# Kernel optimization log

Measured on AMD Instinct MI355X. Metric: run time of the kernel, lower is better.

Reference implementation:

```python
import jax, jax.numpy as jnp
import numpy as np

FS = 50000000.0
PI = jnp.pi


def _scale_matrix(alpha, kW, n_pad):
    """kW x kW matrix equal to torch linear-interp (align_corners=False)
    kW -> N -> kW with N = round(kW / clamp(alpha, 0.001)), N bounded by n_pad."""
    a = jnp.maximum(alpha, 0.001)
    N = jnp.clip(jnp.round(kW / a), 1, n_pad).astype(jnp.int32)
    Nf = N.astype(jnp.float32)
    eye_k = jnp.eye(kW, dtype=jnp.float32)
    eye_n = jnp.eye(n_pad, dtype=jnp.float32)
    # down-sample matrix D: length kW -> N (rows j >= N masked to 0)
    j = jnp.arange(n_pad, dtype=jnp.float32)
    c = jnp.maximum((j + 0.5) * (kW / Nf) - 0.5, 0.0)
    i0f = jnp.floor(c)
    w1 = c - i0f
    i0 = jnp.clip(i0f.astype(jnp.int32), 0, kW - 1)
    i1 = jnp.minimum(i0 + 1, kW - 1)
    D = (1.0 - w1)[:, None] * eye_k[i0] + w1[:, None] * eye_k[i1]
    D = D * (jnp.arange(n_pad) < N)[:, None]
    # up-sample matrix U: length N -> kW (reads only cols < N)
    i = jnp.arange(kW, dtype=jnp.float32)
    c2 = jnp.maximum((i + 0.5) * (Nf / kW) - 0.5, 0.0)
    j0 = jnp.floor(c2).astype(jnp.int32)
    j1 = jnp.minimum(j0 + 1, N - 1)
    w2 = c2 - j0.astype(jnp.float32)
    U = (1.0 - w2)[:, None] * eye_n[j0] + w2[:, None] * eye_n[j1]
    return U @ D  # [kW, kW]


def _mix_phase(w, phi):
    # w: [B,OC,2,1,kW], phi: [B,kW]; complex rotation of (I,Q) channel pair
    I, Q = w[:, :, 0, 0, :], w[:, :, 1, 0, :]
    c, sn = jnp.cos(phi)[:, None, :], jnp.sin(phi)[:, None, :]
    return jnp.stack([I * c - Q * sn, I * sn + Q * c], axis=2)[:, :, :, None, :]


def _steered_kernels(z, s, base_w, B):
    OC, IC, _, kW = base_w.shape
    n_pad = 2 * kW
    sf = jnp.nan_to_num(s)
    act = z > 0
    pick = lambda idx, neutral: jnp.where(act[:, idx], sf[:, idx], neutral)
    wB = jnp.broadcast_to(base_w[None], (B, OC, IC, 1, kW))
    # SCALE (PERTURB_ORDER idx 1)
    alpha = pick(1, 1.0)
    M = jax.vmap(lambda a: _scale_matrix(a, kW, n_pad))(alpha)  # [B,kW,kW]
    wB = jnp.einsum('bij,bocuj->bocui', M, wB)
    # CFO (idx 0) then CHIRP (idx 4): sequential phase rotations = summed phase
    n = jnp.arange(kW, dtype=jnp.float32)
    phi = 2.0 * PI * pick(0, 0.0)[:, None] * n[None, :] / FS
    t = n / FS
    phi = phi + PI * pick(4, 0.0)[:, None] * (t ** 2)[None, :]
    wB = _mix_phase(wB, phi)
    # GAIN (idx 2)
    wB = pick(2, 1.0)[:, None, None, None, None] * wB
    # SHIFT (idx 3): per-sample circular roll, out[i] = in[(i - s) mod kW]
    sh = jnp.round(pick(3, 0.0)).astype(jnp.int32)
    idx = (jnp.arange(kW)[None, :] - sh[:, None]) % kW  # [B,kW]
    idx = jnp.broadcast_to(idx[:, None, None, None, :], wB.shape)
    wB = jnp.take_along_axis(wB, idx, axis=-1)
    return wB  # [B,OC,2,1,kW]


def reference(x, z, s, base_w):
    B, IC, _, L = x.shape
    OC, _, _, kW = base_w.shape
    wB = _steered_kernels(z, s, base_w, B)
    xG = x.reshape(1, B * IC, 1, L)
    wG = wB.reshape(B * OC, IC, 1, kW)
    y = jax.lax.conv_general_dilated(
        xG, wG, window_strides=(1, 1), padding=[(0, 0), (kW // 2, kW // 2)],
        dimension_numbers=('NCHW', 'OIHW', 'NCHW'), feature_group_count=B)
    return y.reshape(B, OC, 1, L)


def setup_inputs() -> dict:
    key = jax.random.key(0)
    ks = jax.random.split(key, 4)
    B, OC, IC, kW, L = 32, 64, 2, 65, 65536
    x = jax.random.normal(ks[0], (B, IC, 1, L), dtype=jnp.float32)
    base_w = jax.random.normal(ks[1], (OC, IC, 1, kW), dtype=jnp.float32) * 0.1
    z = jax.random.randint(ks[2], (B, 5), 0, 2).astype(jnp.int32)
    u = jax.random.uniform(ks[3], (B, 5), dtype=jnp.float32)
    f0 = (u[:, 0] * 2.0 - 1.0) * 1.0e5         # CFO in +/-100 kHz
    alpha = 0.75 + u[:, 1] * 0.65               # SCALE in [0.75, 1.4]
    gain = 0.5 + u[:, 2]                        # GAIN in [0.5, 1.5]
    shift = jnp.round((u[:, 3] * 2.0 - 1.0) * 3.0)  # SHIFT integer in [-3, 3]
    chirp = (u[:, 4] * 2.0 - 1.0) * 1.0e12      # CHIRP rate
    s = jnp.stack([f0, alpha, gain, shift, chirp], axis=1)
    return {"x": x, "z": z, "s": s, "base_w": base_w}
```

## Files before the change

### kernel.cpp

```cpp
#include <hip/hip_runtime.h>
#include <math.h>

#define KW 65
#define L_LEN 65536
#define B_N 32
#define OC_N 64
#define KPAD 160
#define SEC 80
#define LT 256
#define NT 8
#define LGRP (LT*NT)
#define XBASE 344

typedef __attribute__((ext_vector_type(8))) short short8;
typedef __attribute__((ext_vector_type(4))) float f32x4;

__device__ __forceinline__ unsigned short f2bf(float f) {
    unsigned u = __builtin_bit_cast(unsigned, f);
    unsigned r = u + 0x7FFFu + ((u >> 16) & 1u);
    return (unsigned short)(r >> 16);
}

__device__ __forceinline__ float nan0(float v) {
    if (isnan(v)) return 0.0f;
    if (isinf(v)) return v > 0.0f ? 3.4028234663852886e38f : -3.4028234663852886e38f;
    return v;
}

__device__ __forceinline__ void barrier_lds() {
    __builtin_amdgcn_fence(__ATOMIC_RELEASE, "workgroup", "local");
    __builtin_amdgcn_s_barrier();
    __builtin_amdgcn_fence(__ATOMIC_ACQUIRE, "workgroup", "local");
}

__global__ __launch_bounds__(256) void steer_weights(
        const int* __restrict__ z, const float* __restrict__ s,
        const float* __restrict__ bw, unsigned short* __restrict__ wpk) {
    const float PI = 3.14159265358979323846f;
    const float FS = 50000000.0f;
    int b = blockIdx.x;
    int t = threadIdx.x;

    const int*   zb = z + b * 5;
    const float* sb = s + b * 5;
    float f0    = (zb[0] > 0) ? nan0(sb[0]) : 0.0f;
    float alpha = (zb[1] > 0) ? nan0(sb[1]) : 1.0f;
    float gain  = (zb[2] > 0) ? nan0(sb[2]) : 1.0f;
    float shf   = (zb[3] > 0) ? nan0(sb[3]) : 0.0f;
    float chirp = (zb[4] > 0) ? nan0(sb[4]) : 0.0f;

    float a = fmaxf(alpha, 0.001f);
    float Nf_raw = rintf(65.0f / a);
    int   N  = (int)fminf(fmaxf(Nf_raw, 1.0f), 130.0f);
    float Nf = (float)N;
    int   sh = (int)rintf(shf);

    __shared__ float rw[OC_N][2][KW];
    __shared__ float cph[KW], sph[KW];
    __shared__ int   j0t[KW], j1t[KW];
    __shared__ float w2t[KW];
    __shared__ int   i0t[130], i1t[130];
    __shared__ float w1t[130];

    if (t < KW) {
        float n  = (float)t;
        float tt = n / FS;
        float phi = 2.0f * PI * f0 * n / FS + PI * chirp * tt * tt;
        cph[t] = cosf(phi);
        sph[t] = sinf(phi);
        float c2  = fmaxf(((float)t + 0.5f) * (Nf / 65.0f) - 0.5f, 0.0f);
        float j0f = floorf(c2);
        j0t[t] = (int)j0f;
        j1t[t] = min((int)j0f + 1, N - 1);
        w2t[t] = c2 - j0f;
    } else if (t < KW + 130) {
        int j = t - KW;
        float c   = fmaxf(((float)j + 0.5f) * (65.0f / Nf) - 0.5f, 0.0f);
        float i0f = floorf(c);
        int   i0  = min((int)i0f, KW - 1);
        i0t[j] = i0;
        i1t[j] = min(i0 + 1, KW - 1);
        w1t[j] = c - i0f;
    }
    __syncthreads();

    for (int item = t; item < 128 * KW; item += 256) {
        int row = item / KW, i = item % KW;
        const float* w = bw + row * KW;
        int j0 = j0t[i], j1 = j1t[i];
        float v0 = (1.0f - w1t[j0]) * w[i0t[j0]] + w1t[j0] * w[i1t[j0]];
        float v1 = (1.0f - w1t[j1]) * w[i0t[j1]] + w1t[j1] * w[i1t[j1]];
        rw[row >> 1][row & 1][i] = (1.0f - w2t[i]) * v0 + w2t[i] * v1;
    }
    __syncthreads();

    {
        int oc = t >> 2, q = t & 3;
        unsigned short* ob = wpk + ((size_t)b * OC_N + oc) * KPAD;
        int sh0 = ((sh % KW) + KW) % KW;
        int k0 = 17 * q, k1 = min(KW, k0 + 17);
        for (int k = k0; k < k1; ++k) {
            float I = rw[oc][0][k], Q = rw[oc][1][k];
            float cp = cph[k], sp = sph[k];
            float Ip = (I * cp - Q * sp) * gain;
            float Qp = (I * sp + Q * cp) * gain;
            int kk = k + sh0; if (kk >= KW) kk -= KW;
            ob[kk]       = f2bf(Ip);
            ob[SEC + kk] = f2bf(Qp);
        }
        if (q == 3) {
            for (int kk = KW; kk < SEC; ++kk) { ob[kk] = 0; ob[SEC + kk] = 0; }
        }
    }
}

__global__ __launch_bounds__(256, 3) void steer_conv_mfma(
        const float* __restrict__ x, const unsigned short* __restrict__ wpk,
        float* __restrict__ y) {
    int b   = blockIdx.y;
    int L0  = blockIdx.x * LGRP;
    int tid = threadIdx.x;
    int wv = tid >> 6, lane = tid & 63;
    int c = lane & 15, g = lane >> 4;
    int a = wv & 1, lsub = wv >> 1;

    __shared__ __align__(16) unsigned short xt[2][8][2][XBASE];

    short8 afr[2][5];
    #pragma unroll
    for (int ot = 0; ot < 2; ++ot) {
        const unsigned short* wb = wpk + ((size_t)b * OC_N + 32 * a + 16 * ot + c) * KPAD;
        #pragma unroll
        for (int s = 0; s < 5; ++s)
            afr[ot][s] = *(const short8*)(wb + 32 * s + 8 * g);
    }

    const float* xb = x + (size_t)b * 2 * L_LEN;

    bool isLoader = (tid >= 84);
    int lidx = tid - 84;
    int lch = lidx / 86, li4 = lidx % 86;

    int boff[5];
    #pragma unroll
    for (int s = 0; s < 5; ++s) {
        int k0 = 32 * s + 8 * g;
        int ch = (k0 >= SEC) ? 1 : 0;
        int t0 = k0 - SEC * ch;
        boff[s] = ch * XBASE + 128 * lsub + 8 * c + t0;
    }

    auto loadwin = [&](int l0) -> float4 {
        int gi = l0 - 32 + 4 * li4;
        float4 v;
        if (gi >= 0 && gi + 3 < L_LEN) {
            v = *(const float4*)(xb + (size_t)lch * L_LEN + gi);
        } else {
            float tmp[4];
            #pragma unroll
            for (int u = 0; u < 4; ++u) {
                int q = gi + u;
                tmp[u] = (q >= 0 && q < L_LEN) ? xb[(size_t)lch * L_LEN + q] : 0.0f;
            }
            v = make_float4(tmp[0], tmp[1], tmp[2], tmp[3]);
        }
        return v;
    };

    float4 v = make_float4(0.f, 0.f, 0.f, 0.f);
    if (isLoader) v = loadwin(L0);

    int cur = 0;
    for (int t = 0; t < NT; ++t) {
        int l0 = L0 + t * LT;
        if (isLoader) {
            unsigned r0 = (unsigned)f2bf(v.x) | ((unsigned)f2bf(v.y) << 16);
            unsigned r1 = (unsigned)f2bf(v.z) | ((unsigned)f2bf(v.w) << 16);
            *(uint2*)&xt[cur][0][lch][4 * li4] = make_uint2(r0, r1);
        }
        barrier_lds();
        if (tid < 84) {
            int ch = tid / 42, j = tid % 42;
            const unsigned* src = (const unsigned*)&xt[cur][0][ch][8 * j];
            unsigned d[8];
            #pragma unroll
            for (int i = 0; i < 8; ++i) d[i] = src[i];
            #pragma unroll
            for (int p = 1; p < 8; ++p) {
                int q = p >> 1;
                unsigned o[4];
                #pragma unroll
                for (int i = 0; i < 4; ++i)
                    o[i] = (p & 1) ? ((d[i + q] >> 16) | (d[i + q + 1] << 16)) : d[i + q];
                *(uint4*)&xt[cur][p][ch][8 * j] = make_uint4(o[0], o[1], o[2], o[3]);
            }
        } else if (t + 1 < NT) {
            int gi = L0 + (t + 1) * LT - 32 + 4 * li4;
            if (gi >= 0 && gi + 3 < L_LEN) {
                v = loadwin(l0 + LT);
            } else {
                v = loadwin(l0 + LT);
            }
        }
        barrier_lds();

        f32x4 acc[2][8];
        #pragma unroll
        for (int ot = 0; ot < 2; ++ot)
            #pragma unroll
            for (int p = 0; p < 8; ++p) acc[ot][p] = (f32x4){0.f, 0.f, 0.f, 0.f};

        #pragma unroll
        for (int p = 0; p < 8; ++p) {
            const unsigned short* xp = &xt[cur][p][0][0];
            #pragma unroll
            for (int s = 0; s < 5; ++s) {
                short8 bfr = *(const short8*)(xp + boff[s]);
                acc[0][p] = __builtin_amdgcn_mfma_f32_16x16x32_bf16(afr[0][s], bfr, acc[0][p], 0, 0, 0);
                acc[1][p] = __builtin_amdgcn_mfma_f32_16x16x32_bf16(afr[1][s], bfr, acc[1][p], 0, 0, 0);
            }
        }

        #pragma unroll
        for (int ot = 0; ot < 2; ++ot) {
            #pragma unroll
            for (int r = 0; r < 4; ++r) {
                int oc = 32 * a + 16 * ot + 4 * g + r;
                float* yr = y + ((size_t)b * OC_N + oc) * L_LEN + l0 + 128 * lsub + 8 * c;
                f32x4 lo = { acc[ot][0][r], acc[ot][1][r], acc[ot][2][r], acc[ot][3][r] };
                f32x4 hi = { acc[ot][4][r], acc[ot][5][r], acc[ot][6][r], acc[ot][7][r] };
                *(f32x4*)yr       = lo;
                *((f32x4*)yr + 1) = hi;
            }
        }
        cur ^= 1;
    }
}

extern "C" void kernel_launch(void* const* d_in, const int* in_sizes, int n_in,
                              void* d_out, int out_size, void* d_ws, size_t ws_size,
                              hipStream_t stream) {
    const float* x  = (const float*)d_in[0];
    const int*   z  = (const int*)d_in[1];
    const float* s  = (const float*)d_in[2];
    const float* bw = (const float*)d_in[3];
    float* y = (float*)d_out;
    unsigned short* wpk = (unsigned short*)d_ws;

    steer_weights<<<dim3(B_N), dim3(256), 0, stream>>>(z, s, bw, wpk);
    steer_conv_mfma<<<dim3(L_LEN / LGRP, B_N), dim3(256), 0, stream>>>(x, wpk, y);
}
```

Measured before the change: 153.1 us.

## Split weight steering across OC groups and raise conv occupancy bound

The weight-steering kernel now launches 8 blocks per batch, each handling 8 output channels, instead of one block per batch, so more CUs share that prologue work. The conv kernel's launch bounds go from 3 to 4 waves per SIMD, which may force more register pressure or spills. It also replaces the custom LDS-only fence barrier with __syncthreads and adds an interior-block fast path that skips bounds checks on the input loads. Each idea is small on its own, and together they touch both kernels.

```diff
diff --git a/kernel.cpp b/kernel.cpp
--- a/kernel.cpp
+++ b/kernel.cpp
@@ -27,19 +27,14 @@
     return v;
 }
 
-__device__ __forceinline__ void barrier_lds() {
-    __builtin_amdgcn_fence(__ATOMIC_RELEASE, "workgroup", "local");
-    __builtin_amdgcn_s_barrier();
-    __builtin_amdgcn_fence(__ATOMIC_ACQUIRE, "workgroup", "local");
-}
-
 __global__ __launch_bounds__(256) void steer_weights(
         const int* __restrict__ z, const float* __restrict__ s,
         const float* __restrict__ bw, unsigned short* __restrict__ wpk) {
     const float PI = 3.14159265358979323846f;
     const float FS = 50000000.0f;
-    int b = blockIdx.x;
-    int t = threadIdx.x;
+    int ocg = blockIdx.x;
+    int b   = blockIdx.y;
+    int t   = threadIdx.x;
 
     const int*   zb = z + b * 5;
     const float* sb = s + b * 5;
@@ -55,7 +50,7 @@
     float Nf = (float)N;
     int   sh = (int)rintf(shf);
 
-    __shared__ float rw[OC_N][2][KW];
+    __shared__ float rw[8][2][KW];
     __shared__ float cph[KW], sph[KW];
     __shared__ int   j0t[KW], j1t[KW];
     __shared__ float w2t[KW];
@@ -84,9 +79,9 @@
     }
     __syncthreads();
 
-    for (int item = t; item < 128 * KW; item += 256) {
+    for (int item = t; item < 16 * KW; item += 256) {
         int row = item / KW, i = item % KW;
-        const float* w = bw + row * KW;
+        const float* w = bw + (((ocg * 8 + (row >> 1)) * 2) + (row & 1)) * KW;
         int j0 = j0t[i], j1 = j1t[i];
         float v0 = (1.0f - w1t[j0]) * w[i0t[j0]] + w1t[j0] * w[i1t[j0]];
         float v1 = (1.0f - w1t[j1]) * w[i0t[j1]] + w1t[j1] * w[i1t[j1]];
@@ -94,27 +89,27 @@
     }
     __syncthreads();
 
-    {
-        int oc = t >> 2, q = t & 3;
-        unsigned short* ob = wpk + ((size_t)b * OC_N + oc) * KPAD;
-        int sh0 = ((sh % KW) + KW) % KW;
-        int k0 = 17 * q, k1 = min(KW, k0 + 17);
-        for (int k = k0; k < k1; ++k) {
-            float I = rw[oc][0][k], Q = rw[oc][1][k];
-            float cp = cph[k], sp = sph[k];
-            float Ip = (I * cp - Q * sp) * gain;
-            float Qp = (I * sp + Q * cp) * gain;
-            int kk = k + sh0; if (kk >= KW) kk -= KW;
-            ob[kk]       = f2bf(Ip);
-            ob[SEC + kk] = f2bf(Qp);
-        }
-        if (q == 3) {
-            for (int kk = KW; kk < SEC; ++kk) { ob[kk] = 0; ob[SEC + kk] = 0; }
-        }
-    }
-}
-
-__global__ __launch_bounds__(256, 3) void steer_conv_mfma(
+    int sh0 = ((sh % KW) + KW) % KW;
+    for (int item = t; item < 8 * KW; item += 256) {
+        int ocl = item / KW, k = item % KW;
+        unsigned short* ob = wpk + ((size_t)b * OC_N + ocg * 8 + ocl) * KPAD;
+        float I = rw[ocl][0][k], Q = rw[ocl][1][k];
+        float cp = cph[k], sp = sph[k];
+        float Ip = (I * cp - Q * sp) * gain;
+        float Qp = (I * sp + Q * cp) * gain;
+        int kk = k + sh0; if (kk >= KW) kk -= KW;
+        ob[kk]       = f2bf(Ip);
+        ob[SEC + kk] = f2bf(Qp);
+    }
+    for (int item = t; item < 8 * 30; item += 256) {
+        int ocl = item / 30, rem = item % 30;
+        int sec = rem / 15, kk = KW + rem % 15;
+        unsigned short* ob = wpk + ((size_t)b * OC_N + ocg * 8 + ocl) * KPAD;
+        ob[sec * SEC + kk] = 0;
+    }
+}
+
+__global__ __launch_bounds__(256, 4) void steer_conv_mfma(
         const float* __restrict__ x, const unsigned short* __restrict__ wpk,
         float* __restrict__ y) {
     int b   = blockIdx.y;
@@ -135,11 +130,11 @@
             afr[ot][s] = *(const short8*)(wb + 32 * s + 8 * g);
     }
 
-    const float* xb = x + (size_t)b * 2 * L_LEN;
-
     bool isLoader = (tid >= 84);
     int lidx = tid - 84;
     int lch = lidx / 86, li4 = lidx % 86;
+    const float* xrow = x + ((size_t)b * 2 + (isLoader ? lch : 0)) * L_LEN;
+    bool interior = (L0 >= 32) && (L0 + LGRP - 32 + 4 * 85 + 3 < L_LEN);
 
     int boff[5];
     #pragma unroll
@@ -152,19 +147,15 @@
 
     auto loadwin = [&](int l0) -> float4 {
         int gi = l0 - 32 + 4 * li4;
-        float4 v;
-        if (gi >= 0 && gi + 3 < L_LEN) {
-            v = *(const float4*)(xb + (size_t)lch * L_LEN + gi);
-        } else {
-            float tmp[4];
-            #pragma unroll
-            for (int u = 0; u < 4; ++u) {
-                int q = gi + u;
-                tmp[u] = (q >= 0 && q < L_LEN) ? xb[(size_t)lch * L_LEN + q] : 0.0f;
-            }
-            v = make_float4(tmp[0], tmp[1], tmp[2], tmp[3]);
-        }
-        return v;
+        if (interior || (gi >= 0 && gi + 3 < L_LEN))
+            return *(const float4*)(xrow + gi);
+        float tmp[4];
+        #pragma unroll
+        for (int u = 0; u < 4; ++u) {
+            int q = gi + u;
+            tmp[u] = (q >= 0 && q < L_LEN) ? xrow[q] : 0.0f;
+        }
+        return make_float4(tmp[0], tmp[1], tmp[2], tmp[3]);
     };
 
     float4 v = make_float4(0.f, 0.f, 0.f, 0.f);
@@ -178,7 +169,7 @@
             unsigned r1 = (unsigned)f2bf(v.z) | ((unsigned)f2bf(v.w) << 16);
             *(uint2*)&xt[cur][0][lch][4 * li4] = make_uint2(r0, r1);
         }
-        barrier_lds();
+        __syncthreads();
         if (tid < 84) {
             int ch = tid / 42, j = tid % 42;
             const unsigned* src = (const unsigned*)&xt[cur][0][ch][8 * j];
@@ -195,14 +186,9 @@
                 *(uint4*)&xt[cur][p][ch][8 * j] = make_uint4(o[0], o[1], o[2], o[3]);
             }
         } else if (t + 1 < NT) {
-            int gi = L0 + (t + 1) * LT - 32 + 4 * li4;
-            if (gi >= 0 && gi + 3 < L_LEN) {
-                v = loadwin(l0 + LT);
-            } else {
-                v = loadwin(l0 + LT);
-            }
-        }
-        barrier_lds();
+            v = loadwin(l0 + LT);
+        }
+        __syncthreads();
 
         f32x4 acc[2][8];
         #pragma unroll
@@ -247,6 +233,6 @@
     float* y = (float*)d_out;
     unsigned short* wpk = (unsigned short*)d_ws;
 
-    steer_weights<<<dim3(B_N), dim3(256), 0, stream>>>(z, s, bw, wpk);
+    steer_weights<<<dim3(8, B_N), dim3(256), 0, stream>>>(z, s, bw, wpk);
     steer_conv_mfma<<<dim3(L_LEN / LGRP, B_N), dim3(256), 0, stream>>>(x, wpk, y);
 }
```

After: 188.5 us. +23.1%, slower.
